# Kernel optimization log

Measured on AMD Instinct MI355X. Metric: run time of the kernel, lower is better.

## Reference

```python
import jax, jax.numpy as jnp
import numpy as np

IN, H1, H2 = 118, 256, 128
EPS = 1e-5

def _linear_init(key, out_f, in_f):
    k1, k2 = jax.random.split(key)
    bound = 1.0 / np.sqrt(in_f)
    W = jax.random.uniform(k1, (out_f, in_f), minval=-bound, maxval=bound, dtype=jnp.float32)
    b = jax.random.uniform(k2, (out_f,), minval=-bound, maxval=bound, dtype=jnp.float32)
    return W, b

def setup_inputs() -> dict:
    key = jax.random.key(0)
    ks = jax.random.split(key, 10)
    x = jax.random.normal(ks[0], (512, 512, IN), dtype=jnp.float32)
    Wf1, bf1 = _linear_init(ks[1], H1, IN + H1)
    Wi1, bi1 = _linear_init(ks[2], H1, IN + H1)
    Wg1, bg1 = _linear_init(ks[3], H1, IN + H1)
    Wo1, bo1 = _linear_init(ks[4], H1, IN + H1)
    Wf2, bf2 = _linear_init(ks[5], H2, H1 + H2)
    Wi2, bi2 = _linear_init(ks[6], H2, H1 + H2)
    Wg2, bg2 = _linear_init(ks[7], H2, H1 + H2)
    Wo2, bo2 = _linear_init(ks[8], H2, H1 + H2)
    gamma1 = jnp.ones((H1,), jnp.float32); beta1 = jnp.zeros((H1,), jnp.float32)
    gamma2 = jnp.ones((H2,), jnp.float32); beta2 = jnp.zeros((H2,), jnp.float32)
    return dict(x=x, Wf1=Wf1, Wi1=Wi1, Wg1=Wg1, Wo1=Wo1, bf1=bf1, bi1=bi1, bg1=bg1, bo1=bo1,
                Wf2=Wf2, Wi2=Wi2, Wg2=Wg2, Wo2=Wo2, bf2=bf2, bi2=bi2, bg2=bg2, bo2=bo2,
                gamma1=gamma1, beta1=beta1, gamma2=gamma2, beta2=beta2)

def _layernorm(h, g, b):
    mu = jnp.mean(h, axis=-1, keepdims=True)
    var = jnp.mean(jnp.square(h - mu), axis=-1, keepdims=True)
    return (h - mu) * jax.lax.rsqrt(var + EPS) * g + b

def _lstm_step(comb, W, b, c_prev, H):
    # W: [4H, in+H] stacked (f,i,g,o). One fused GEMM, then split.
    z = comb @ W.T + b  # [B, 4H]
    f = jax.nn.sigmoid(z[:, 0*H:1*H])
    i = jax.nn.sigmoid(z[:, 1*H:2*H])
    g = jnp.tanh(z[:, 2*H:3*H])
    o = jax.nn.sigmoid(z[:, 3*H:4*H])
    c = f * c_prev + i * g
    h = o * jnp.tanh(c)
    return h, c

def reference(x, Wf1, Wi1, Wg1, Wo1, bf1, bi1, bg1, bo1,
              Wf2, Wi2, Wg2, Wo2, bf2, bi2, bg2, bo2,
              gamma1, beta1, gamma2, beta2):
    B, S, _ = x.shape
    W1 = jnp.concatenate([Wf1, Wi1, Wg1, Wo1], axis=0)  # [4*H1, IN+H1]
    b1 = jnp.concatenate([bf1, bi1, bg1, bo1], axis=0)
    W2 = jnp.concatenate([Wf2, Wi2, Wg2, Wo2], axis=0)  # [4*H2, H1+H2]
    b2 = jnp.concatenate([bf2, bi2, bg2, bo2], axis=0)

    def step(carry, x_t):
        h1, c1, h2, c2 = carry
        h1n, c1n = _lstm_step(jnp.concatenate([x_t, h1], axis=1), W1, b1, c1, H1)
        h1n = _layernorm(h1n, gamma1, beta1)  # dropout is identity in eval
        h2n, c2n = _lstm_step(jnp.concatenate([h1n, h2], axis=1), W2, b2, c2, H2)
        h2n = _layernorm(h2n, gamma2, beta2)
        return (h1n, c1n, h2n, c2n), None

    init = (jnp.zeros((B, H1), x.dtype), jnp.zeros((B, H1), x.dtype),
            jnp.zeros((B, H2), x.dtype), jnp.zeros((B, H2), x.dtype))
    (h1, c1, h2, c2), _ = jax.lax.scan(step, init, jnp.swapaxes(x, 0, 1))
    return h2
```

## Files before the change

kernel.cpp:

```cpp
#include <hip/hip_runtime.h>
#include <hip/hip_fp16.h>
#include <stdint.h>

#define B_  512
#define S_  512
#define IN_ 118
#define H1_ 256
#define H2_ 128

#define NT_  16
#define NS1_ 8
#define NS2_ 4
#define NBLK (NT_*(NS1_+NS2_))

#define WSCALE    1024.0f
#define WSCALE_I  0.0009765625f

typedef __attribute__((ext_vector_type(8))) short frag8;
typedef __attribute__((ext_vector_type(4))) float facc4;
typedef unsigned short u16;
typedef unsigned int   u32;

#define OFF_W1H 0
#define OFF_W1L 786432
#define OFF_W2H 1572864
#define OFF_W2L 1966080
#define OFF_AR1 2359296
#define OFF_AR2 (OFF_AR1 + 8192)
#define OFF_DN2 (OFF_AR2 + 4096)
#define OFF_REG (OFF_AR1 + 16384)
#define OFF_HX  (OFF_AR1 + 65536)

#define A1IDX(bt,bs) ((((bt)*8+(bs))<<4))
#define A2IDX(bt,vs) ((((bt)*4+(vs))<<4))

#define GETREG_XCC 63508

__device__ __forceinline__ void splitf(float v, u16& hi, u16& lo) {
    __half h = __float2half(v);
    float hf = __half2float(h);
    __half l = __float2half(v - hf);
    hi = *(u16*)&h; lo = *(u16*)&l;
}

__device__ __forceinline__ float exp_(float x) {
    const float A  = 1.44269504f;
    const float Ae = 1.9259630e-8f;
    float a = x * A;
    float e = __builtin_fmaf(x, A, -a);
    e = __builtin_fmaf(x, Ae, e);
    float p;
    asm("v_exp_f32 %0, %1" : "=v"(p) : "v"(a));
    return __builtin_fmaf(p * 0.69314718f, e, p);
}
__device__ __forceinline__ float sigm_(float x) {
    return 1.f / (1.f + exp_(fmaxf(-x, -88.f)));
}
__device__ __forceinline__ float tanh_(float x) {
    float ax = fabsf(x);
    float e  = exp_(-2.f * ax);
    float r  = (1.f - e) / (1.f + e);
    return copysignf(r, x);
}
__device__ __forceinline__ float rsqrt_(float x) {
    float r = rsqrtf(x);
    return r * __builtin_fmaf(-0.5f * x, r * r, 1.5f);
}

__device__ __forceinline__ u32 ld_flag(const u32* p) {
    return __hip_atomic_load(p, __ATOMIC_RELAXED, __HIP_MEMORY_SCOPE_AGENT);
}
__device__ __forceinline__ void st_flag(u32* p, u32 v) {
    __hip_atomic_store(p, v, __ATOMIC_RELAXED, __HIP_MEMORY_SCOPE_AGENT);
}
__device__ __forceinline__ float ld_coh(const float* p) {
    return __hip_atomic_load(p, __ATOMIC_RELAXED, __HIP_MEMORY_SCOPE_AGENT);
}
__device__ __forceinline__ void st_coh(float* p, float v) {
    __hip_atomic_store(p, v, __ATOMIC_RELAXED, __HIP_MEMORY_SCOPE_AGENT);
}
__device__ __forceinline__ void l1_inv() {
    asm volatile("s_waitcnt vmcnt(0)\n\tbuffer_inv sc0" ::: "memory");
}

__global__ void prep_weights(const float* __restrict__ Wf1, const float* __restrict__ Wi1,
                             const float* __restrict__ Wg1, const float* __restrict__ Wo1,
                             const float* __restrict__ Wf2, const float* __restrict__ Wi2,
                             const float* __restrict__ Wg2, const float* __restrict__ Wo2,
                             u16* __restrict__ w1h, u16* __restrict__ w1l,
                             u16* __restrict__ w2h, u16* __restrict__ w2l) {
    int idx = blockIdx.x * 256 + threadIdx.x;
    if (idx >= 589824) return;
    if (idx < 393216) {
        int j  = idx & 7;
        int L  = (idx >> 3) & 63;
        int fr = idx >> 9;
        int kf = fr % 12, tile = fr / 12;
        int bs = tile >> 3, ln = tile & 7;
        int khat = kf*32 + (L >> 4)*8 + j;
        int lc   = ln*16 + (L & 15);
        int g = lc >> 5, unit = bs*32 + (lc & 31);
        const float* Wg[4] = {Wf1, Wi1, Wg1, Wo1};
        float v = 0.f;
        if (khat < IN_)       v = Wg[g][unit*374 + khat];
        else if (khat >= 128) v = Wg[g][unit*374 + khat - 10];
        v *= WSCALE;
        u16 hi, lo; splitf(v, hi, lo);
        w1h[idx] = hi; w1l[idx] = lo;
    } else {
        int i2 = idx - 393216;
        int j  = i2 & 7;
        int L  = (i2 >> 3) & 63;
        int fr = i2 >> 9;
        int kf = fr % 12, tile = fr / 12;
        int vs = tile >> 3, ln = tile & 7;
        int khat = kf*32 + (L >> 4)*8 + j;
        int lc   = ln*16 + (L & 15);
        int g = lc >> 5, unit = vs*32 + (lc & 31);
        const float* Wg[4] = {Wf2, Wi2, Wg2, Wo2};
        float v = Wg[g][unit*384 + khat] * WSCALE;
        u16 hi, lo; splitf(v, hi, lo);
        w2h[i2] = hi; w2l[i2] = lo;
    }
}


template<int NC>
__device__ __forceinline__ void build_ln(u16* combH, u16* combL, int lds_c0,
    const float* __restrict__ src, int Hstr, float invH,
    const float* sG, const float* sB, int tid, int zero, int fast)
{
    int row = tid >> 4, tc = tid & 15;
    if (tc >= 8) return;
    if (!zero) {
        const float* p = src + (size_t)row*Hstr;
        float v[NC];
        if (fast) {
            #pragma unroll
            for (int g8 = 0; g8 < NC/8; ++g8)
                #pragma unroll
                for (int j = 0; j < 8; ++j)
                    v[g8*8+j] = p[g8*64 + tc*8 + j];
        } else {
            #pragma unroll
            for (int g8 = 0; g8 < NC/8; ++g8)
                #pragma unroll
                for (int j = 0; j < 8; ++j)
                    v[g8*8+j] = ld_coh(&p[g8*64 + tc*8 + j]);
        }
        float p4[NC/4];
        #pragma unroll
        for (int j = 0; j < NC/4; ++j)
            p4[j] = (v[4*j] + v[4*j+1]) + (v[4*j+2] + v[4*j+3]);
        #pragma unroll
        for (int st = 1; st < NC/4; st <<= 1)
            #pragma unroll
            for (int j = 0; j < NC/4; j += 2*st) p4[j] += p4[j+st];
        float s = p4[0];
        #pragma unroll
        for (int off = 1; off < 8; off <<= 1) s += __shfl_xor(s, off, 64);
        float mu = s * invH;
        #pragma unroll
        for (int j = 0; j < NC/4; ++j) {
            float d0 = v[4*j]   - mu, d1 = v[4*j+1] - mu;
            float d2 = v[4*j+2] - mu, d3 = v[4*j+3] - mu;
            p4[j] = (d0*d0 + d1*d1) + (d2*d2 + d3*d3);
        }
        #pragma unroll
        for (int st = 1; st < NC/4; st <<= 1)
            #pragma unroll
            for (int j = 0; j < NC/4; j += 2*st) p4[j] += p4[j+st];
        float sq = p4[0];
        #pragma unroll
        for (int off = 1; off < 8; off <<= 1) sq += __shfl_xor(sq, off, 64);
        float rs = rsqrt_(__builtin_fmaf(sq, invH, 1e-5f));
        #pragma unroll
        for (int g8 = 0; g8 < NC/8; ++g8) {
            frag8 fh, fl;
            #pragma unroll
            for (int j = 0; j < 8; ++j) {
                int u = g8*64 + tc*8 + j;
                float t_ = (v[g8*8+j] - mu)*rs;
                float hn = __builtin_fmaf(t_, sG[u], sB[u]);
                u16 hi, lo; splitf(hn, hi, lo);
                fh[j] = (short)hi; fl[j] = (short)lo;
            }
            *(frag8*)&combH[row*392 + lds_c0 + g8*64 + tc*8] = fh;
            *(frag8*)&combL[row*392 + lds_c0 + g8*64 + tc*8] = fl;
        }
    } else {
        frag8 z = {0,0,0,0,0,0,0,0};
        #pragma unroll
        for (int g8 = 0; g8 < NC/8; ++g8) {
            *(frag8*)&combH[row*392 + lds_c0 + g8*64 + tc*8] = z;
            *(frag8*)&combL[row*392 + lds_c0 + g8*64 + tc*8] = z;
        }
    }
}

template<int KF0, int KF1>
__device__ __forceinline__ void gemm_part(const u16* combH, const u16* combL,
    const frag8 (&wH)[12], const frag8 (&wL)[12], int lane, facc4 (&acc)[2])
{
    const int q = lane >> 4, cc = lane & 15;
    #pragma unroll
    for (int kf = KF0; kf < KF1; ++kf) {
        #pragma unroll
        for (int m = 0; m < 2; ++m) {
            frag8 aH = *(const frag8*)&combH[(m*16+cc)*392 + kf*32 + q*8];
            frag8 aL = *(const frag8*)&combL[(m*16+cc)*392 + kf*32 + q*8];
            acc[m] = __builtin_amdgcn_mfma_f32_16x16x32_f16(aH, wH[kf], acc[m], 0, 0, 0);
            acc[m] = __builtin_amdgcn_mfma_f32_16x16x32_f16(aL, wH[kf], acc[m], 0, 0, 0);
            acc[m] = __builtin_amdgcn_mfma_f32_16x16x32_f16(aL, wL[kf], acc[m], 0, 0, 0);
            acc[m] = __builtin_amdgcn_mfma_f32_16x16x32_f16(aH, wL[kf], acc[m], 0, 0, 0);
        }
    }
}

__device__ __forceinline__ void zdump8(u16* combH, u16* combL, int w, int lane,
                                       const facc4 (&acc)[2], int zoff)
{
    const int q = lane >> 4, cc = lane & 15;
    float* zp = (w < 4) ? (float*)combH : (float*)combL;
    int lcl = ((w & 3)*16) + cc;
    #pragma unroll
    for (int m = 0; m < 2; ++m)
        #pragma unroll
        for (int r = 0; r < 4; ++r)
            zp[(m*16 + q*4 + r)*196 + zoff + lcl] = acc[m][r];
}

__device__ __forceinline__ void gates_update8(const u16* combH, const u16* combL,
    const float* bz, float* cst, int tid, float* houtBase, int Hstr, int zoff, int fast)
{
    const float* zH = (const float*)combH + zoff;
    const float* zL = (const float*)combL + zoff;
    const int u = tid & 31, rb = tid >> 5;
    const float bzf = bz[u], bzi = bz[32+u], bzg = bz[64+u], bzo = bz[96+u];
    #pragma unroll
    for (int rr = 0; rr < 2; ++rr) {
        int row = rr*16 + rb;
        float zf = __builtin_fmaf(zH[row*196 + u],      WSCALE_I, bzf);
        float zi = __builtin_fmaf(zH[row*196 + 32 + u], WSCALE_I, bzi);
        float zg = __builtin_fmaf(zL[row*196 + u],      WSCALE_I, bzg);
        float zo = __builtin_fmaf(zL[row*196 + 32 + u], WSCALE_I, bzo);
        float ig = sigm_(zi) * tanh_(zg);
        float c  = __builtin_fmaf(sigm_(zf), cst[rr], ig);
        cst[rr]  = c;
        float hv = sigm_(zo)*tanh_(c);
        if (fast) houtBase[(size_t)row*Hstr + u] = hv;
        else      st_coh(&houtBase[(size_t)row*Hstr + u], hv);
    }
}

__device__ __forceinline__ void xprefetch(const float* __restrict__ x, int b0,
                                          int t, int tid, float (&xv)[8])
{
    int row = tid >> 4, tc = tid & 15;
    const float* xp = &x[((size_t)(b0+row)*S_ + t)*IN_];
    #pragma unroll
    for (int j = 0; j < 8; ++j) {
        int col = tc*8 + j;
        xv[j] = (col < IN_) ? xp[col] : 0.f;
    }
}

__global__ __launch_bounds__(512, 2) void lstm_seq(
    const float* __restrict__ x,
    const float* __restrict__ bf1, const float* __restrict__ bi1,
    const float* __restrict__ bg1, const float* __restrict__ bo1,
    const float* __restrict__ bf2, const float* __restrict__ bi2,
    const float* __restrict__ bg2, const float* __restrict__ bo2,
    const float* __restrict__ gamma1, const float* __restrict__ beta1,
    const float* __restrict__ gamma2, const float* __restrict__ beta2,
    const u16* __restrict__ w1h, const u16* __restrict__ w1l,
    const u16* __restrict__ w2h, const u16* __restrict__ w2l,
    float* __restrict__ h1x, float* __restrict__ h2x,
    u32* __restrict__ a1, u32* __restrict__ a2, u32* __restrict__ dn2,
    u32* __restrict__ regx, int R, float* __restrict__ out)
{
    extern __shared__ char smem[];
    u16*   combH = (u16*)smem;
    u16*   combL = (u16*)(smem + 25088);
    float* fA    = (float*)(smem + 50176);
    int*   sFast = (int*)(smem + 53760);
    const int tid  = threadIdx.x;
    const int w    = tid >> 6;
    const int lane = tid & 63;

    const int bhw  = blockIdx.x;
    const int xcd  = bhw & 7, slot = bhw >> 3;
    const int grp  = (slot >= 12) ? 1 : 0;
    const int sl   = slot - grp*12;
    const int bt   = xcd + 8*grp;
    const int b0   = bt * 32;

    if (tid == 0) {
        u32 myx = ((u32)__builtin_amdgcn_s_getreg(GETREG_XCC)) & 15u;
        st_flag(&regx[bhw], myx + 1u);
        u32 x0 = 0; int ok = 1;
        #pragma unroll 1
        for (int r = 0; r < 12; ++r) {
            int mb = 8*(grp*12 + r) + xcd;
            u32 v; do { v = ld_flag(&regx[mb]); } while (v == 0u);
            if (r == 0) x0 = v; else ok &= (v == x0);
        }
        *sFast = ok;
    }

    if (sl < 8) {
        const int bs = sl;
        float* bz = fA;
        float* sG = fA + 128;
        float* sB = fA + 384;
        if (tid < 128) {
            int g = tid >> 5, unit = bs*32 + (tid & 31);
            const float* bp = (g==0)?bf1:(g==1)?bi1:(g==2)?bg1:bo1;
            bz[tid] = bp[unit];
        }
        if (tid < 256) { sG[tid] = gamma1[tid]; sB[tid] = beta1[tid]; }
        frag8 wH[12], wL[12];
        #pragma unroll
        for (int kf = 0; kf < 12; ++kf) {
            size_t base = ((((size_t)bs*8 + w)*12 + kf)*64 + lane)*8;
            wH[kf] = *(const frag8*)&w1h[base];
            wL[kf] = *(const frag8*)&w1l[base];
        }
        float cst[2] = {0.f, 0.f};
        float xv[8];
        xprefetch(x, b0, 0, tid, xv);
        __syncthreads();
        const int fast = *sFast;

        int slotW = 0, slotR = 0;
        for (int t = 0; t < S_; ++t) {
            {
                int row = tid >> 4, tc = tid & 15;
                frag8 fh, fl;
                #pragma unroll
                for (int j = 0; j < 8; ++j) {
                    u16 hi, lo; splitf(xv[j], hi, lo);
                    fh[j] = (short)hi; fl[j] = (short)lo;
                }
                *(frag8*)&combH[row*392 + tc*8] = fh;
                *(frag8*)&combL[row*392 + tc*8] = fl;
            }
            __syncthreads();
            facc4 acc[2];
            acc[0] = (facc4){0.f,0.f,0.f,0.f}; acc[1] = (facc4){0.f,0.f,0.f,0.f};
            gemm_part<0,4>(combH, combL, wH, wL, lane, acc);
            {
                u32 need = 0; u32* p = nullptr;
                if (tid < 8 && t > 0)                    { p = &a1[A1IDX(bt, tid)];    need = (u32)t; }
                else if (tid >= 8 && tid < 12 && t >= R) { p = &dn2[A2IDX(bt, tid-8)]; need = (u32)(t - R + 1); }
                if (need) while (ld_flag(p) < need) {}
            }
            __syncthreads();
            if (fast) l1_inv();
            build_ln<32>(combH, combL, 128, &h1x[((size_t)slotR*B_ + b0)*H1_], H1_,
                         1.f/H1_, sG, sB, tid, t == 0, fast);
            __syncthreads();
            gemm_part<4,12>(combH, combL, wH, wL, lane, acc);
            zdump8(combH, combL, w, lane, acc, 0);
            __syncthreads();
            gates_update8(combH, combL, bz, cst, tid,
                          &h1x[((size_t)slotW*B_ + b0)*H1_ + bs*32], H1_, 0, fast);
            if (t + 1 < S_) xprefetch(x, b0, t+1, tid, xv);
            __syncthreads();
            if (tid == 0) st_flag(&a1[A1IDX(bt, bs)], (u32)(t + 1));
            slotR = slotW; slotW = (slotW + 1 == R) ? 0 : slotW + 1;
        }
    } else {
        const int vs = sl - 8;
        float* bz  = fA;
        float* sG1 = fA + 128;
        float* sB1 = fA + 384;
        float* sG2 = fA + 640;
        float* sB2 = fA + 768;
        if (tid < 128) {
            int g = tid >> 5, unit = vs*32 + (tid & 31);
            const float* bp = (g==0)?bf2:(g==1)?bi2:(g==2)?bg2:bo2;
            bz[tid] = bp[unit];
        }
        if (tid < 256) { sG1[tid] = gamma1[tid]; sB1[tid] = beta1[tid]; }
        if (tid < 128) { sG2[tid] = gamma2[tid]; sB2[tid] = beta2[tid]; }
        frag8 wH[12], wL[12];
        #pragma unroll
        for (int kf = 0; kf < 12; ++kf) {
            size_t base = ((((size_t)vs*8 + w)*12 + kf)*64 + lane)*8;
            wH[kf] = *(const frag8*)&w2h[base];
            wL[kf] = *(const frag8*)&w2l[base];
        }
        float cst[2] = {0.f, 0.f};
        __syncthreads();
        const int fast = *sFast;

        int slotW = 0, slotR = 0, slot1 = 0;
        for (int t = 0; t < S_; ++t) {
            if (tid < 4 && t > 0) { u32* p = &a2[A2IDX(bt, tid)]; while (ld_flag(p) < (u32)t) {} }
            __syncthreads();
            if (fast) l1_inv();
            build_ln<16>(combH, combL, 256, &h2x[((size_t)slotR*B_ + b0)*H2_], H2_,
                         1.f/H2_, sG2, sB2, tid, t == 0, fast);
            if (tid < 8) { u32* p = &a1[A1IDX(bt, tid)]; while (ld_flag(p) < (u32)(t+1)) {} }
            __syncthreads();
            if (fast) l1_inv();
            build_ln<32>(combH, combL, 0, &h1x[((size_t)slot1*B_ + b0)*H1_], H1_,
                         1.f/H1_, sG1, sB1, tid, 0, fast);
            __syncthreads();
            if (tid == 0) st_flag(&dn2[A2IDX(bt, vs)], (u32)(t + 1));
            facc4 acc[2];
            acc[0] = (facc4){0.f,0.f,0.f,0.f}; acc[1] = (facc4){0.f,0.f,0.f,0.f};
            gemm_part<0,12>(combH, combL, wH, wL, lane, acc);
            __syncthreads();
            zdump8(combH, combL, w, lane, acc, 128);
            __syncthreads();
            gates_update8(combH, combL, bz, cst, tid,
                          &h2x[((size_t)slotW*B_ + b0)*H2_ + vs*32], H2_, 128, fast);
            __syncthreads();
            if (tid == 0) st_flag(&a2[A2IDX(bt, vs)], (u32)(t + 1));
            slotR = slotW; slotW = (slotW + 1 == R) ? 0 : slotW + 1;
            slot1 = (slot1 + 1 == R) ? 0 : slot1 + 1;
        }
        if (vs == 0) {
            if (tid < 4) { u32* p = &a2[A2IDX(bt, tid)]; while (ld_flag(p) < (u32)S_) {} }
            __syncthreads();
            int row = tid >> 4, tc = tid & 15;
            if (tc < 8) {
                const float* p = &h2x[((size_t)slotR*B_ + b0 + row)*H2_];
                float v[16];
                #pragma unroll
                for (int g8 = 0; g8 < 2; ++g8)
                    #pragma unroll
                    for (int j = 0; j < 8; ++j)
                        v[g8*8+j] = ld_coh(&p[g8*64 + tc*8 + j]);
                float p4[4];
                #pragma unroll
                for (int j = 0; j < 4; ++j)
                    p4[j] = (v[4*j] + v[4*j+1]) + (v[4*j+2] + v[4*j+3]);
                float s = (p4[0] + p4[1]) + (p4[2] + p4[3]);
                #pragma unroll
                for (int off = 1; off < 8; off <<= 1) s += __shfl_xor(s, off, 64);
                float mu = s * (1.f/H2_);
                #pragma unroll
                for (int j = 0; j < 4; ++j) {
                    float d0 = v[4*j]   - mu, d1 = v[4*j+1] - mu;
                    float d2 = v[4*j+2] - mu, d3 = v[4*j+3] - mu;
                    p4[j] = (d0*d0 + d1*d1) + (d2*d2 + d3*d3);
                }
                float sq = (p4[0] + p4[1]) + (p4[2] + p4[3]);
                #pragma unroll
                for (int off = 1; off < 8; off <<= 1) sq += __shfl_xor(sq, off, 64);
                float rs = rsqrt_(__builtin_fmaf(sq, 1.f/H2_, 1e-5f));
                #pragma unroll
                for (int g8 = 0; g8 < 2; ++g8)
                    #pragma unroll
                    for (int j = 0; j < 8; ++j) {
                        int u = g8*64 + tc*8 + j;
                        float t_ = (v[g8*8+j]-mu)*rs;
                        out[((size_t)(b0+row))*H2_ + u] = __builtin_fmaf(t_, sG2[u], sB2[u]);
                    }
            }
        }
    }
}

extern "C" void kernel_launch(void* const* d_in, const int* in_sizes, int n_in,
                              void* d_out, int out_size, void* d_ws, size_t ws_size,
                              hipStream_t stream) {
    const float* x      = (const float*)d_in[0];
    const float* Wf1    = (const float*)d_in[1];
    const float* Wi1    = (const float*)d_in[2];
    const float* Wg1    = (const float*)d_in[3];
    const float* Wo1    = (const float*)d_in[4];
    const float* bf1    = (const float*)d_in[5];
    const float* bi1    = (const float*)d_in[6];
    const float* bg1    = (const float*)d_in[7];
    const float* bo1    = (const float*)d_in[8];
    const float* Wf2    = (const float*)d_in[9];
    const float* Wi2    = (const float*)d_in[10];
    const float* Wg2    = (const float*)d_in[11];
    const float* Wo2    = (const float*)d_in[12];
    const float* bf2    = (const float*)d_in[13];
    const float* bi2    = (const float*)d_in[14];
    const float* bg2    = (const float*)d_in[15];
    const float* bo2    = (const float*)d_in[16];
    const float* gamma1 = (const float*)d_in[17];
    const float* beta1  = (const float*)d_in[18];
    const float* gamma2 = (const float*)d_in[19];
    const float* beta2  = (const float*)d_in[20];

    char* ws = (char*)d_ws;
    u16* w1h = (u16*)(ws + OFF_W1H);
    u16* w1l = (u16*)(ws + OFF_W1L);
    u16* w2h = (u16*)(ws + OFF_W2H);
    u16* w2l = (u16*)(ws + OFF_W2L);
    u32* a1  = (u32*)(ws + OFF_AR1);
    u32* a2  = (u32*)(ws + OFF_AR2);
    u32* dn2 = (u32*)(ws + OFF_DN2);
    u32* regx= (u32*)(ws + OFF_REG);

    int R = (int)((ws_size - OFF_HX) / 786432);
    if (R > 16) R = 16;
    if (R < 2)  R = 2;
    float* h1x = (float*)(ws + OFF_HX);
    float* h2x = (float*)(ws + OFF_HX + (size_t)R * 524288);

    hipMemsetAsync(ws + OFF_AR1, 0, 65536, stream);

    prep_weights<<<2304, 256, 0, stream>>>(Wf1, Wi1, Wg1, Wo1, Wf2, Wi2, Wg2, Wo2,
                                           w1h, w1l, w2h, w2l);

    lstm_seq<<<dim3(NBLK), dim3(512), 53776, stream>>>(
        x, bf1, bi1, bg1, bo1, bf2, bi2, bg2, bo2,
        gamma1, beta1, gamma2, beta2,
        w1h, w1l, w2h, w2l,
        h1x, h2x, a1, a2, dn2, regx,
        R, (float*)d_out);
}
```

Baseline: 3.650 ms.

## Interleave gate columns and compute LSTM gates in registers via lane shuffles

The packed weight and bias layout now interleaves the four gates per unit (f,i,g,o adjacent), so each MFMA output tile holds all four gates of a unit in neighbouring lanes. Gates are then computed straight from the accumulators with wave shuffles, which removes the LDS z dump and two block barriers per timestep in both layers. The x tile for the next step is also built during the layer-1 LN phase, and its load is prefetched two steps ahead, taking one more barrier off the critical path. The cost is redundant sigmoid/tanh work in the three of every four lanes that do not store, plus eight cell-state registers per thread instead of two.

```diff
diff --git a/kernel.cpp b/kernel.cpp
--- a/kernel.cpp
+++ b/kernel.cpp
@@ -99,7 +99,7 @@
         int bs = tile >> 3, ln = tile & 7;
         int khat = kf*32 + (L >> 4)*8 + j;
         int lc   = ln*16 + (L & 15);
-        int g = lc >> 5, unit = bs*32 + (lc & 31);
+        int g = lc & 3, unit = bs*32 + (lc >> 2);
         const float* Wg[4] = {Wf1, Wi1, Wg1, Wo1};
         float v = 0.f;
         if (khat < IN_)       v = Wg[g][unit*374 + khat];
@@ -116,7 +116,7 @@
         int vs = tile >> 3, ln = tile & 7;
         int khat = kf*32 + (L >> 4)*8 + j;
         int lc   = ln*16 + (L & 15);
-        int g = lc >> 5, unit = vs*32 + (lc & 31);
+        int g = lc & 3, unit = vs*32 + (lc >> 2);
         const float* Wg[4] = {Wf2, Wi2, Wg2, Wo2};
         float v = Wg[g][unit*384 + khat] * WSCALE;
         u16 hi, lo; splitf(v, hi, lo);
@@ -217,40 +217,33 @@
     }
 }
 
-__device__ __forceinline__ void zdump8(u16* combH, u16* combL, int w, int lane,
-                                       const facc4 (&acc)[2], int zoff)
+__device__ __forceinline__ void gates_inreg(const facc4 (&acc)[2], const float* bz,
+    float (&cst)[8], int w, int lane, float* houtBase, int Hstr, int fast)
 {
     const int q = lane >> 4, cc = lane & 15;
-    float* zp = (w < 4) ? (float*)combH : (float*)combL;
-    int lcl = ((w & 3)*16) + cc;
+    const int ubase = lane & 60;
+    const int colb = w*16 + (cc & 12);
+    const float bzf = bz[colb+0], bzi = bz[colb+1], bzg = bz[colb+2], bzo = bz[colb+3];
+    const int ul = w*4 + (cc >> 2);
     #pragma unroll
     for (int m = 0; m < 2; ++m)
         #pragma unroll
-        for (int r = 0; r < 4; ++r)
-            zp[(m*16 + q*4 + r)*196 + zoff + lcl] = acc[m][r];
-}
-
-__device__ __forceinline__ void gates_update8(const u16* combH, const u16* combL,
-    const float* bz, float* cst, int tid, float* houtBase, int Hstr, int zoff, int fast)
-{
-    const float* zH = (const float*)combH + zoff;
-    const float* zL = (const float*)combL + zoff;
-    const int u = tid & 31, rb = tid >> 5;
-    const float bzf = bz[u], bzi = bz[32+u], bzg = bz[64+u], bzo = bz[96+u];
-    #pragma unroll
-    for (int rr = 0; rr < 2; ++rr) {
-        int row = rr*16 + rb;
-        float zf = __builtin_fmaf(zH[row*196 + u],      WSCALE_I, bzf);
-        float zi = __builtin_fmaf(zH[row*196 + 32 + u], WSCALE_I, bzi);
-        float zg = __builtin_fmaf(zL[row*196 + u],      WSCALE_I, bzg);
-        float zo = __builtin_fmaf(zL[row*196 + 32 + u], WSCALE_I, bzo);
-        float ig = sigm_(zi) * tanh_(zg);
-        float c  = __builtin_fmaf(sigm_(zf), cst[rr], ig);
-        cst[rr]  = c;
-        float hv = sigm_(zo)*tanh_(c);
-        if (fast) houtBase[(size_t)row*Hstr + u] = hv;
-        else      st_coh(&houtBase[(size_t)row*Hstr + u], hv);
-    }
+        for (int r = 0; r < 4; ++r) {
+            float z  = acc[m][r];
+            float zf = __builtin_fmaf(__shfl(z, ubase+0, 64), WSCALE_I, bzf);
+            float zi = __builtin_fmaf(__shfl(z, ubase+1, 64), WSCALE_I, bzi);
+            float zg = __builtin_fmaf(__shfl(z, ubase+2, 64), WSCALE_I, bzg);
+            float zo = __builtin_fmaf(__shfl(z, ubase+3, 64), WSCALE_I, bzo);
+            float ig = sigm_(zi) * tanh_(zg);
+            float c  = __builtin_fmaf(sigm_(zf), cst[m*4+r], ig);
+            cst[m*4+r] = c;
+            float hv = sigm_(zo)*tanh_(c);
+            if ((cc & 3) == 0) {
+                int row = m*16 + q*4 + r;
+                if (fast) houtBase[(size_t)row*Hstr + ul] = hv;
+                else      st_coh(&houtBase[(size_t)row*Hstr + ul], hv);
+            }
+        }
 }
 
 __device__ __forceinline__ void xprefetch(const float* __restrict__ x, int b0,
@@ -263,6 +256,20 @@
         int col = tc*8 + j;
         xv[j] = (col < IN_) ? xp[col] : 0.f;
     }
+}
+
+__device__ __forceinline__ void xbuild(u16* combH, u16* combL, int tid,
+                                       const float (&xv)[8])
+{
+    int row = tid >> 4, tc = tid & 15;
+    frag8 fh, fl;
+    #pragma unroll
+    for (int j = 0; j < 8; ++j) {
+        u16 hi, lo; splitf(xv[j], hi, lo);
+        fh[j] = (short)hi; fl[j] = (short)lo;
+    }
+    *(frag8*)&combH[row*392 + tc*8] = fh;
+    *(frag8*)&combL[row*392 + tc*8] = fl;
 }
 
 __global__ __launch_bounds__(512, 2) void lstm_seq(
@@ -314,7 +321,7 @@
         float* sG = fA + 128;
         float* sB = fA + 384;
         if (tid < 128) {
-            int g = tid >> 5, unit = bs*32 + (tid & 31);
+            int g = tid & 3, unit = bs*32 + (tid >> 2);
             const float* bp = (g==0)?bf1:(g==1)?bi1:(g==2)?bg1:bo1;
             bz[tid] = bp[unit];
         }
@@ -326,26 +333,17 @@
             wH[kf] = *(const frag8*)&w1h[base];
             wL[kf] = *(const frag8*)&w1l[base];
         }
-        float cst[2] = {0.f, 0.f};
+        float cst[8] = {0.f,0.f,0.f,0.f,0.f,0.f,0.f,0.f};
         float xv[8];
         xprefetch(x, b0, 0, tid, xv);
         __syncthreads();
         const int fast = *sFast;
+        xbuild(combH, combL, tid, xv);
+        xprefetch(x, b0, 1, tid, xv);
+        __syncthreads();
 
         int slotW = 0, slotR = 0;
         for (int t = 0; t < S_; ++t) {
-            {
-                int row = tid >> 4, tc = tid & 15;
-                frag8 fh, fl;
-                #pragma unroll
-                for (int j = 0; j < 8; ++j) {
-                    u16 hi, lo; splitf(xv[j], hi, lo);
-                    fh[j] = (short)hi; fl[j] = (short)lo;
-                }
-                *(frag8*)&combH[row*392 + tc*8] = fh;
-                *(frag8*)&combL[row*392 + tc*8] = fl;
-            }
-            __syncthreads();
             facc4 acc[2];
             acc[0] = (facc4){0.f,0.f,0.f,0.f}; acc[1] = (facc4){0.f,0.f,0.f,0.f};
             gemm_part<0,4>(combH, combL, wH, wL, lane, acc);
@@ -359,13 +357,12 @@
             if (fast) l1_inv();
             build_ln<32>(combH, combL, 128, &h1x[((size_t)slotR*B_ + b0)*H1_], H1_,
                          1.f/H1_, sG, sB, tid, t == 0, fast);
+            if (t + 1 < S_) xbuild(combH, combL, tid, xv);
             __syncthreads();
             gemm_part<4,12>(combH, combL, wH, wL, lane, acc);
-            zdump8(combH, combL, w, lane, acc, 0);
-            __syncthreads();
-            gates_update8(combH, combL, bz, cst, tid,
-                          &h1x[((size_t)slotW*B_ + b0)*H1_ + bs*32], H1_, 0, fast);
-            if (t + 1 < S_) xprefetch(x, b0, t+1, tid, xv);
+            gates_inreg(acc, bz, cst, w, lane,
+                        &h1x[((size_t)slotW*B_ + b0)*H1_ + bs*32], H1_, fast);
+            if (t + 2 < S_) xprefetch(x, b0, t+2, tid, xv);
             __syncthreads();
             if (tid == 0) st_flag(&a1[A1IDX(bt, bs)], (u32)(t + 1));
             slotR = slotW; slotW = (slotW + 1 == R) ? 0 : slotW + 1;
@@ -378,7 +375,7 @@
         float* sG2 = fA + 640;
         float* sB2 = fA + 768;
         if (tid < 128) {
-            int g = tid >> 5, unit = vs*32 + (tid & 31);
+            int g = tid & 3, unit = vs*32 + (tid >> 2);
             const float* bp = (g==0)?bf2:(g==1)?bi2:(g==2)?bg2:bo2;
             bz[tid] = bp[unit];
         }
@@ -391,7 +388,7 @@
             wH[kf] = *(const frag8*)&w2h[base];
             wL[kf] = *(const frag8*)&w2l[base];
         }
-        float cst[2] = {0.f, 0.f};
+        float cst[8] = {0.f,0.f,0.f,0.f,0.f,0.f,0.f,0.f};
         __syncthreads();
         const int fast = *sFast;
 
@@ -412,11 +409,8 @@
             facc4 acc[2];
             acc[0] = (facc4){0.f,0.f,0.f,0.f}; acc[1] = (facc4){0.f,0.f,0.f,0.f};
             gemm_part<0,12>(combH, combL, wH, wL, lane, acc);
-            __syncthreads();
-            zdump8(combH, combL, w, lane, acc, 128);
-            __syncthreads();
-            gates_update8(combH, combL, bz, cst, tid,
-                          &h2x[((size_t)slotW*B_ + b0)*H2_ + vs*32], H2_, 128, fast);
+            gates_inreg(acc, bz, cst, w, lane,
+                        &h2x[((size_t)slotW*B_ + b0)*H2_ + vs*32], H2_, fast);
             __syncthreads();
             if (tid == 0) st_flag(&a2[A2IDX(bt, vs)], (u32)(t + 1));
             slotR = slotW; slotW = (slotW + 1 == R) ? 0 : slotW + 1;
```

Measured after the change: 4.712 ms. 29.1% more time.
